# Performance work log

Measured on AMD Instinct MI355X. Metric: run time of the kernel, lower is better.

## Reference

```python
import jax, jax.numpy as jnp
import numpy as np
from jax import lax

B, N, HID = 2, 1024, 2048
H, D, HKV = 32, 64, 8
GROUPS = H // HKV
CHUNK = 64
MAG = 0.5
GATE_NORM = 16.0


def setup_inputs() -> dict:
    key = jax.random.key(0)
    ks = jax.random.split(key, 5)
    hidden_states = jax.random.normal(ks[0], (B, N, HID), jnp.float32)
    Wq = jax.random.normal(ks[1], (HID, H * D), jnp.float32) * 0.02
    Wk = jax.random.normal(ks[2], (HID, HKV * D), jnp.float32) * 0.02
    Wv = jax.random.normal(ks[3], (HID, HKV * D), jnp.float32) * 0.02
    Wo = jax.random.normal(ks[4], (H * D, HID), jnp.float32) * 0.02
    return {"hidden_states": hidden_states, "Wq": Wq, "Wk": Wk, "Wv": Wv, "Wo": Wo}


def _repeat_kv(x, g):
    # [b, hkv, n, d] -> [b, hkv*g, n, d]
    return jnp.repeat(x, g, axis=1)


def _delta_rule_chunked(q, k, v, beta, chunk):
    """Chunked delta-rule linear attention (DeltaNet-style) with elementwise beta gate."""
    b, h, n, d = q.shape
    nc = n // chunk
    qc, kc, vc, bc = (x.reshape(b, h, nc, chunk, d) for x in (q, k, v, beta))
    k_beta = kc * bc
    v_beta = vc * bc
    # T = (I + tril(k_beta k^T, -1))^{-1}, a unit lower-triangular solve per chunk
    strict = jnp.tril(jnp.ones((chunk, chunk), bool), -1)
    L = jnp.einsum('bhnid,bhnjd->bhnij', k_beta, kc) * strict
    M = L + jnp.eye(chunk, dtype=q.dtype)
    eye = jnp.broadcast_to(jnp.eye(chunk, dtype=q.dtype), M.shape)
    T = jax.scipy.linalg.solve_triangular(M, eye, lower=True, unit_diagonal=True)
    u = jnp.einsum('bhnij,bhnjd->bhnid', T, v_beta)   # pseudo-values
    w = jnp.einsum('bhnij,bhnjd->bhnid', T, k_beta)   # pseudo-keys
    causal = jnp.tril(jnp.ones((chunk, chunk), bool))

    def step(S, xs):
        qi, ki, ui, wi = xs  # each [b, h, chunk, d]; S: [b, h, d, d]
        u_p = ui - jnp.einsum('bhcd,bhde->bhce', wi, S)
        attn = jnp.einsum('bhid,bhjd->bhij', qi, ki) * causal
        o = jnp.einsum('bhcd,bhde->bhce', qi, S) + jnp.einsum('bhij,bhjd->bhid', attn, u_p)
        S_new = S + jnp.einsum('bhcd,bhce->bhde', ki, u_p)
        return S_new, o

    xs = tuple(jnp.moveaxis(x, 2, 0) for x in (qc, kc, u, w))  # [nc, b, h, chunk, d]
    S0 = jnp.zeros((b, h, d, d), q.dtype)
    S_final, o = lax.scan(step, S0, xs)
    o = jnp.moveaxis(o, 0, 2).reshape(b, h, n, d)
    return o, S_final


def reference(hidden_states, Wq, Wk, Wv, Wo):
    b, n, _ = hidden_states.shape
    q = hidden_states @ Wq            # [b, n, H*D]
    k = hidden_states @ Wk            # [b, n, HKV*D]
    v = hidden_states @ Wv            # [b, n, HKV*D]
    g = k  # AdaptiveAvgPool1d(512 -> 512) is the identity here

    qh = q.reshape(b, n, H, D).transpose(0, 2, 1, 3)      # [b, H, n, D]
    kh = k.reshape(b, n, HKV, D).transpose(0, 2, 1, 3)    # [b, HKV, n, D]
    vh = v.reshape(b, n, HKV, D).transpose(0, 2, 1, 3)
    gh = g.reshape(b, n, HKV, D).transpose(0, 2, 1, 3)
    k_rep = _repeat_kv(kh, GROUPS)
    v_rep = _repeat_kv(vh, GROUPS)
    g_rep = _repeat_kv(gh, GROUPS)

    # linear-attention branch: softmax feature maps + log-sigmoid gate
    ql = jax.nn.softmax(qh, axis=-1).astype(jnp.float32)
    kl = jax.nn.softmax(k_rep, axis=-1).astype(jnp.float32)
    gl = (jax.nn.log_sigmoid(g_rep) / GATE_NORM).astype(jnp.float32)
    o_lin, _ = _delta_rule_chunked(ql, kl, v_rep.astype(jnp.float32), gl, CHUNK)
    o_lin = o_lin.transpose(0, 2, 1, 3).reshape(b, n, H * D) @ Wo

    # base (vanilla causal) attention branch
    scale = 1.0 / np.sqrt(D).astype(np.float32)
    scores = jnp.einsum('bhid,bhjd->bhij', qh, k_rep) * scale
    causal = jnp.tril(jnp.ones((n, n), bool))
    scores = jnp.where(causal, scores, jnp.finfo(scores.dtype).min)
    attn_weights = jax.nn.softmax(scores, axis=-1)
    o_base = jnp.einsum('bhij,bhjd->bhid', attn_weights, v_rep)
    o_base = o_base.transpose(0, 2, 1, 3).reshape(b, n, H * D) @ Wo

    out = MAG * o_lin + (1.0 - MAG) * o_base
    return out, attn_weights
```

## Files before the change

kernel.cpp:

```cpp
#include <hip/hip_runtime.h>
#include <hip/hip_bf16.h>

constexpr int Bc = 2, Nc = 1024, HIDc = 2048, Hc = 32, Dc = 64, HKVc = 8, NCc = 16;

typedef unsigned short bfu;
typedef __attribute__((ext_vector_type(8))) short frag_ab;
typedef __attribute__((ext_vector_type(4))) float frag_cd;

__device__ __forceinline__ bfu f2bf(float f) {
  unsigned int u = __float_as_uint(f);
  unsigned int r = u + 0x7fffu + ((u >> 16) & 1u);
  return (bfu)(r >> 16);
}
__device__ __forceinline__ ushort4 pack4(float4 v) {
  ushort4 r; r.x = f2bf(v.x); r.y = f2bf(v.y); r.z = f2bf(v.z); r.w = f2bf(v.w);
  return r;
}

__device__ __forceinline__ void gl16(const bfu* g, bfu* l) {
  __builtin_amdgcn_global_load_lds(
      (const __attribute__((address_space(1))) void*)g,
      (__attribute__((address_space(3))) void*)l, 16, 0, 0);
}

__global__ __launch_bounds__(256) void cast_bf16_k(
    const float* __restrict__ in, bfu* __restrict__ out)
{
  const size_t i = ((size_t)blockIdx.x * 256 + threadIdx.x) * 4;
  *(ushort4*)(out + i) = pack4(*(const float4*)(in + i));
}

__global__ __launch_bounds__(256) void transpose_cast_k(
    const float* __restrict__ W, bfu* __restrict__ WT, int K, int N)
{
  __shared__ float t[32][33];
  const int bn = blockIdx.x * 32, bk = blockIdx.y * 32;
  const int x = threadIdx.x & 31, y = threadIdx.x >> 5;
#pragma unroll
  for (int i = 0; i < 32; i += 8)
    t[y + i][x] = W[(size_t)(bk + y + i) * N + bn + x];
  __syncthreads();
#pragma unroll
  for (int i = 0; i < 32; i += 8)
    WT[(size_t)(bn + y + i) * K + bk + x] = f2bf(t[x][y + i]);
}

__global__ __launch_bounds__(256) void transpose_v_k(
    const float* __restrict__ v, bfu* __restrict__ vt)
{
  __shared__ __align__(16) bfu T[64][72];
  const int blk = blockIdx.x;
  const int nt = blk & 15, bh = blk >> 4;
  const int hk = bh & 7, b = bh >> 3;
  const int tid = threadIdx.x;
  const int n = tid >> 2, dv0 = (tid & 3) * 16;
  const float* src = v + ((size_t)(b * Nc + nt * 64 + n) * 8 + hk) * 64 + dv0;
#pragma unroll
  for (int e = 0; e < 16; ++e) T[dv0 + e][n] = f2bf(src[e]);
  __syncthreads();
  const int r = tid >> 3, c = (tid & 7) * 8;
#pragma unroll
  for (int hh = 0; hh < 2; ++hh) {
    const int dv = r + hh * 32;
    *(uint4*)(vt + ((size_t)(bh * 64 + dv)) * 1024 + nt * 64 + c) =
        *(const uint4*)&T[dv][c];
  }
}

__device__ __forceinline__ void gemm128_gl(
    const bfu* __restrict__ A, const bfu* __restrict__ BT,
    float* __restrict__ C, const int Nn, const int m0, const int n0,
    bfu* As, bfu* Bs)
{
  const int tid = threadIdx.x;
  const int wave = tid >> 6, lane = tid & 63;
  const int wm = (wave >> 1) * 64, wn = (wave & 1) * 64;
  const int fm = lane & 15, quad = lane >> 4;
  const int sr = tid >> 2, skc = (tid & 3) * 8;

  frag_cd acc[4][4];
#pragma unroll
  for (int i = 0; i < 4; ++i)
#pragma unroll
    for (int j = 0; j < 4; ++j) acc[i][j] = (frag_cd){0.f, 0.f, 0.f, 0.f};

  const bfu* Ag = A + (size_t)(m0 + sr) * 2048 + skc;
  const bfu* Bg = BT + (size_t)(n0 + sr) * 2048 + skc;
  bfu* Al = As + tid * 8;
  bfu* Bl = Bs + tid * 8;

  for (int k0 = 0; k0 < 2048; k0 += 32) {
    gl16(Ag + k0, Al);
    gl16(Ag + k0 + (size_t)64 * 2048, Al + 64 * 32);
    gl16(Bg + k0, Bl);
    gl16(Bg + k0 + (size_t)64 * 2048, Bl + 64 * 32);
    __syncthreads();
    frag_ab a[4], b[4];
#pragma unroll
    for (int im = 0; im < 4; ++im)
      a[im] = *(const frag_ab*)&As[(size_t)(wm + im * 16 + fm) * 32 + quad * 8];
#pragma unroll
    for (int in = 0; in < 4; ++in)
      b[in] = *(const frag_ab*)&Bs[(size_t)(wn + in * 16 + fm) * 32 + quad * 8];
#pragma unroll
    for (int im = 0; im < 4; ++im)
#pragma unroll
      for (int in = 0; in < 4; ++in)
        acc[im][in] = __builtin_amdgcn_mfma_f32_16x16x32_bf16(
            a[im], b[in], acc[im][in], 0, 0, 0);
    __syncthreads();
  }
#pragma unroll
  for (int im = 0; im < 4; ++im)
#pragma unroll
    for (int in = 0; in < 4; ++in) {
      const int n = n0 + wn + in * 16 + fm;
#pragma unroll
      for (int r = 0; r < 4; ++r) {
        const int m = m0 + wm + im * 16 + quad * 4 + r;
        C[(size_t)m * Nn + n] = acc[im][in][r];
      }
    }
}

__global__ __launch_bounds__(256) void gemm_qkv_k(
    const bfu* __restrict__ A, const bfu* __restrict__ BTq,
    const bfu* __restrict__ BTk, const bfu* __restrict__ BTv,
    float* __restrict__ Cq, float* __restrict__ Ck, float* __restrict__ Cv)
{
  __shared__ __align__(16) bfu As[128 * 32];
  __shared__ __align__(16) bfu Bs[128 * 32];
  int bx = blockIdx.x;
  const bfu* BT; float* C; int Nn;
  if (bx < 16)      { BT = BTq; C = Cq; Nn = 2048; }
  else if (bx < 20) { BT = BTk; C = Ck; Nn = 512; bx -= 16; }
  else              { BT = BTv; C = Cv; Nn = 512; bx -= 20; }
  gemm128_gl(A, BT, C, Nn, blockIdx.y * 128, bx * 128, As, Bs);
}

__global__ __launch_bounds__(256) void gemm_wo_k(
    const bfu* __restrict__ A, const bfu* __restrict__ BT, float* __restrict__ C)
{
  __shared__ __align__(16) bfu As[128 * 32];
  __shared__ __align__(16) bfu Bs[128 * 32];
  gemm128_gl(A, BT, C, 2048, blockIdx.y * 128, blockIdx.x * 128, As, Bs);
}

__global__ __launch_bounds__(256) void gates64_k(
    const float* __restrict__ kin, float* __restrict__ kl, float* __restrict__ gl,
    bfu* __restrict__ k_bf)
{
  const int r = blockIdx.x * 4 + (threadIdx.x >> 6);
  const int lane = threadIdx.x & 63;
  const size_t idx = (size_t)r * 64 + lane;
  const float x = kin[idx];
  k_bf[idx] = f2bf(x);
  float m = x;
#pragma unroll
  for (int o = 32; o > 0; o >>= 1) m = fmaxf(m, __shfl_xor(m, o, 64));
  const float e = __expf(x - m);
  float s = e;
#pragma unroll
  for (int o = 32; o > 0; o >>= 1) s += __shfl_xor(s, o, 64);
  kl[idx] = e / s;
  const float ls = fminf(x, 0.f) - log1pf(__expf(-fabsf(x)));
  gl[idx] = ls * 0.0625f;
}

__global__ __launch_bounds__(256) void chunk_prep_k(
    const float* __restrict__ kl, const float* __restrict__ v,
    const float* __restrict__ gl, float* __restrict__ u_out, float* __restrict__ w_out)
{
  __shared__ __align__(16) float KC[64][68];
  __shared__ float KB[64][65];
  __shared__ float VB[64][65];
  const int blk = blockIdx.x;
  const int c = blk & 15, bh = blk >> 4;
  const int hk = bh & 7, b = bh >> 3;
  const int tid = threadIdx.x;
  for (int x = tid; x < 4096; x += 256) {
    const int i = x >> 6, d = x & 63;
    const size_t src = ((size_t)(b * Nc + c * 64 + i) * 8 + hk) * 64 + d;
    const float kv = kl[src], g = gl[src], vv = v[src];
    KC[d][i] = kv; KB[i][d] = kv * g; VB[i][d] = vv * g;
  }
  __syncthreads();
  const int li = tid >> 2, j0 = (tid & 3) * 16;
  float acc[16];
#pragma unroll
  for (int jj = 0; jj < 16; ++jj) acc[jj] = 0.f;
  for (int d = 0; d < 64; ++d) {
    const float kb = KB[li][d];
    const float4 c0v = *(const float4*)&KC[d][j0];
    const float4 c1v = *(const float4*)&KC[d][j0 + 4];
    const float4 c2v = *(const float4*)&KC[d][j0 + 8];
    const float4 c3v = *(const float4*)&KC[d][j0 + 12];
    acc[0] += kb * c0v.x;  acc[1] += kb * c0v.y;  acc[2] += kb * c0v.z;  acc[3] += kb * c0v.w;
    acc[4] += kb * c1v.x;  acc[5] += kb * c1v.y;  acc[6] += kb * c1v.z;  acc[7] += kb * c1v.w;
    acc[8] += kb * c2v.x;  acc[9] += kb * c2v.y;  acc[10] += kb * c2v.z; acc[11] += kb * c2v.w;
    acc[12] += kb * c3v.x; acc[13] += kb * c3v.y; acc[14] += kb * c3v.z; acc[15] += kb * c3v.w;
  }
  __syncthreads();
#pragma unroll
  for (int jj = 0; jj < 16; ++jj)
    KC[li][j0 + jj] = (j0 + jj < li) ? acc[jj] : 0.f;
  __syncthreads();
  if (tid < 128) {
    const int d = tid & 63;
    float (*X)[65] = (tid < 64) ? VB : KB;
    for (int i = 1; i < 64; ++i) {
      float a2 = X[i][d];
      for (int j = 0; j < i; ++j) a2 -= KC[i][j] * X[j][d];
      X[i][d] = a2;
    }
  }
  __syncthreads();
  for (int x = tid; x < 4096; x += 256) {
    u_out[(size_t)blk * 4096 + x] = VB[x >> 6][x & 63];
    w_out[(size_t)blk * 4096 + x] = KB[x >> 6][x & 63];
  }
}

__global__ __launch_bounds__(512) void scan_k(
    const float* __restrict__ u_ps, const float* __restrict__ w_ps,
    const float* __restrict__ kl, float* __restrict__ u_p, float* __restrict__ S_pre)
{
  __shared__ __align__(16) float S[64][68];
  __shared__ __align__(16) float kw[64][68];
  __shared__ __align__(16) float kt[64][68];
  __shared__ __align__(16) float up[64][68];
  const int blk = blockIdx.x;
  const int hk = blk & 7, b = blk >> 3;
  const int t = threadIdx.x;
  const int row = t >> 3;
  const int c0 = (t & 7) * 8;
  for (int x = t; x < 4096; x += 512) S[x >> 6][x & 63] = 0.f;
  __syncthreads();
  for (int c = 0; c < 16; ++c) {
    const size_t cb = ((size_t)blk * 16 + c) * 4096;
    float upre[8];
    {
      const float* ug = u_ps + cb + row * 64 + c0;
#pragma unroll
      for (int j = 0; j < 8; ++j) upre[j] = ug[j];
    }
    for (int x = t; x < 4096; x += 512) {
      const int i = x >> 6, d = x & 63;
      S_pre[cb + x] = S[i][d];
      kw[i][d] = w_ps[cb + x];
      kt[i][d] = kl[((size_t)(b * Nc + c * 64 + i) * 8 + hk) * 64 + d];
    }
    __syncthreads();
    {
      float acc[8];
#pragma unroll
      for (int j = 0; j < 8; ++j) acc[j] = upre[j];
      for (int e4 = 0; e4 < 64; e4 += 4) {
        const float4 wv4 = *(const float4*)&kw[row][e4];
#pragma unroll
        for (int ee = 0; ee < 4; ++ee) {
          const float wv = ((const float*)&wv4)[ee];
          const float4 s0 = *(const float4*)&S[e4 + ee][c0];
          const float4 s1 = *(const float4*)&S[e4 + ee][c0 + 4];
          acc[0] -= wv * s0.x; acc[1] -= wv * s0.y;
          acc[2] -= wv * s0.z; acc[3] -= wv * s0.w;
          acc[4] -= wv * s1.x; acc[5] -= wv * s1.y;
          acc[6] -= wv * s1.z; acc[7] -= wv * s1.w;
        }
      }
      const float4 o0 = make_float4(acc[0], acc[1], acc[2], acc[3]);
      const float4 o1 = make_float4(acc[4], acc[5], acc[6], acc[7]);
      *(float4*)&up[row][c0] = o0;
      *(float4*)&up[row][c0 + 4] = o1;
      float* upg = u_p + cb + row * 64 + c0;
      *(float4*)upg = o0;
      *(float4*)(upg + 4) = o1;
    }
    __syncthreads();
    {
      float sacc[8];
      {
        const float4 s0 = *(const float4*)&S[row][c0];
        const float4 s1 = *(const float4*)&S[row][c0 + 4];
        sacc[0] = s0.x; sacc[1] = s0.y; sacc[2] = s0.z; sacc[3] = s0.w;
        sacc[4] = s1.x; sacc[5] = s1.y; sacc[6] = s1.z; sacc[7] = s1.w;
      }
      for (int i = 0; i < 64; ++i) {
        const float kv = kt[i][row];
        const float4 u0 = *(const float4*)&up[i][c0];
        const float4 u1 = *(const float4*)&up[i][c0 + 4];
        sacc[0] += kv * u0.x; sacc[1] += kv * u0.y;
        sacc[2] += kv * u0.z; sacc[3] += kv * u0.w;
        sacc[4] += kv * u1.x; sacc[5] += kv * u1.y;
        sacc[6] += kv * u1.z; sacc[7] += kv * u1.w;
      }
      *(float4*)&S[row][c0] = make_float4(sacc[0], sacc[1], sacc[2], sacc[3]);
      *(float4*)&S[row][c0 + 4] = make_float4(sacc[4], sacc[5], sacc[6], sacc[7]);
    }
    __syncthreads();
  }
}

__global__ __launch_bounds__(256) void olin_k(
    const float* __restrict__ qraw, const float* __restrict__ kl,
    const float* __restrict__ upb, const float* __restrict__ S_pre,
    float* __restrict__ o_comb)
{
  __shared__ float Q[64][65];
  __shared__ __align__(16) float Bb[64][68];
  __shared__ float At[64][65];
  const int blk = blockIdx.x;
  const int c = blk & 15, bh = blk >> 4;
  const int h = bh & 31, b = bh >> 5, hk = h >> 2;
  const int tid = threadIdx.x;
  const int i = tid >> 2, d0 = (tid & 3) * 16;
  for (int x = tid; x < 4096; x += 256) {
    const int r = x >> 6, d = x & 63;
    Q[r][d] = qraw[((size_t)(b * Nc + c * 64 + r) * 32 + h) * 64 + d];
    Bb[d][r] = kl[((size_t)(b * Nc + c * 64 + r) * 8 + hk) * 64 + d];
  }
  __syncthreads();
  {
    float mx = -1e30f;
#pragma unroll
    for (int j = 0; j < 16; ++j) mx = fmaxf(mx, Q[i][d0 + j]);
#pragma unroll
    for (int o = 1; o < 4; o <<= 1) mx = fmaxf(mx, __shfl_xor(mx, o, 64));
    float ev[16];
    float sum = 0.f;
#pragma unroll
    for (int j = 0; j < 16; ++j) { ev[j] = __expf(Q[i][d0 + j] - mx); sum += ev[j]; }
#pragma unroll
    for (int o = 1; o < 4; o <<= 1) sum += __shfl_xor(sum, o, 64);
    const float inv = 1.f / sum;
#pragma unroll
    for (int j = 0; j < 16; ++j) Q[i][d0 + j] = ev[j] * inv;
  }
  __syncthreads();
  {
    float a[16];
#pragma unroll
    for (int j = 0; j < 16; ++j) a[j] = 0.f;
    for (int d = 0; d < 64; ++d) {
      const float qv = Q[i][d];
      const float4 b0 = *(const float4*)&Bb[d][d0];
      const float4 b1 = *(const float4*)&Bb[d][d0 + 4];
      const float4 b2 = *(const float4*)&Bb[d][d0 + 8];
      const float4 b3 = *(const float4*)&Bb[d][d0 + 12];
      a[0] += qv * b0.x;  a[1] += qv * b0.y;  a[2] += qv * b0.z;  a[3] += qv * b0.w;
      a[4] += qv * b1.x;  a[5] += qv * b1.y;  a[6] += qv * b1.z;  a[7] += qv * b1.w;
      a[8] += qv * b2.x;  a[9] += qv * b2.y;  a[10] += qv * b2.z; a[11] += qv * b2.w;
      a[12] += qv * b3.x; a[13] += qv * b3.y; a[14] += qv * b3.z; a[15] += qv * b3.w;
    }
#pragma unroll
    for (int j = 0; j < 16; ++j) At[i][d0 + j] = (d0 + j <= i) ? a[j] : 0.f;
  }
  __syncthreads();
  const size_t cb = ((size_t)(b * 8 + hk) * 16 + c) * 4096;
  for (int x = tid; x < 4096; x += 256) Bb[x >> 6][x & 63] = S_pre[cb + x];
  __syncthreads();
  float o[16];
#pragma unroll
  for (int j = 0; j < 16; ++j) o[j] = 0.f;
  for (int e = 0; e < 64; ++e) {
    const float qv = Q[i][e];
#pragma unroll
    for (int j = 0; j < 16; ++j) o[j] += qv * Bb[e][d0 + j];
  }
  __syncthreads();
  for (int x = tid; x < 4096; x += 256) Bb[x >> 6][x & 63] = upb[cb + x];
  __syncthreads();
  for (int j2 = 0; j2 < 64; ++j2) {
    const float av = At[i][j2];
#pragma unroll
    for (int j = 0; j < 16; ++j) o[j] += av * Bb[j2][d0 + j];
  }
  float* oc = o_comb + ((size_t)(b * Nc + c * 64 + i) * 32 + h) * 64 + d0;
#pragma unroll
  for (int j = 0; j < 16; ++j) oc[j] = 0.5f * o[j];
}

template <int LDK>
__device__ __forceinline__ void stage_tile(
    const bfu* __restrict__ g, size_t row_stride, bfu* dst, int tid)
{
  const int xr = tid >> 3;
  const int xc = (tid & 7) * 8;
#pragma unroll
  for (int hh = 0; hh < 2; ++hh) {
    const int row = xr + hh * 32;
    *(uint4*)&dst[(size_t)row * LDK + xc] =
        *(const uint4*)(g + (size_t)row * row_stride + xc);
  }
}

__global__ __launch_bounds__(256) void ml_mfma_k(
    const bfu* __restrict__ qbf, const bfu* __restrict__ kbf,
    float* __restrict__ mbuf, float* __restrict__ lbuf)
{
  constexpr int LDK = 72;
  __shared__ __align__(16) bfu Qt[64 * LDK];
  __shared__ __align__(16) bfu Kt[64 * LDK];
  __shared__ float mred[4][64];
  __shared__ float lred[4][64];
  const int blk = blockIdx.x;
  const int ib = blk & 15, bh = blk >> 4;
  const int h = bh & 31, b = bh >> 5, hk = h >> 2;
  const int tid = threadIdx.x;
  const int wave = tid >> 6, lane = tid & 63;
  const int fm = lane & 15, quad = lane >> 4;
  const int wj = wave * 16;

  stage_tile<LDK>(qbf + ((size_t)(b * Nc + ib * 64) * 32 + h) * 64,
                  (size_t)32 * 64, Qt, tid);
  __syncthreads();
  frag_ab qb[4][2];
#pragma unroll
  for (int in = 0; in < 4; ++in)
#pragma unroll
    for (int kk = 0; kk < 2; ++kk)
      qb[in][kk] = *(const frag_ab*)&Qt[(size_t)(in * 16 + fm) * LDK + kk * 32 + quad * 8];

  float m[4], l[4];
#pragma unroll
  for (int in = 0; in < 4; ++in) { m[in] = -1e30f; l[in] = 0.f; }

  for (int jt = 0; jt <= ib; ++jt) {
    __syncthreads();
    stage_tile<LDK>(kbf + ((size_t)(b * Nc + jt * 64) * 8 + hk) * 64,
                    (size_t)8 * 64, Kt, tid);
    __syncthreads();
    frag_ab ka[2];
    ka[0] = *(const frag_ab*)&Kt[(size_t)(wj + fm) * LDK + quad * 8];
    ka[1] = *(const frag_ab*)&Kt[(size_t)(wj + fm) * LDK + 32 + quad * 8];
    const bool diag = (jt == ib);
#pragma unroll
    for (int in = 0; in < 4; ++in) {
      frag_cd acc = (frag_cd){0.f, 0.f, 0.f, 0.f};
      acc = __builtin_amdgcn_mfma_f32_16x16x32_bf16(ka[0], qb[in][0], acc, 0, 0, 0);
      acc = __builtin_amdgcn_mfma_f32_16x16x32_bf16(ka[1], qb[in][1], acc, 0, 0, 0);
      const int iloc = in * 16 + fm;
      float sv[4];
      bool vd[4];
      float tm = -1e30f;
#pragma unroll
      for (int r = 0; r < 4; ++r) {
        const int jloc = wj + quad * 4 + r;
        vd[r] = !diag || (jloc <= iloc);
        sv[r] = acc[r] * 0.125f;
        if (vd[r]) tm = fmaxf(tm, sv[r]);
      }
      const float mn = fmaxf(m[in], tm);
      float lsum = 0.f;
#pragma unroll
      for (int r = 0; r < 4; ++r)
        if (vd[r]) lsum += __expf(sv[r] - mn);
      l[in] = l[in] * __expf(m[in] - mn) + lsum;
      m[in] = mn;
    }
  }
#pragma unroll
  for (int in = 0; in < 4; ++in) {
    float mm = m[in], ll = l[in];
#pragma unroll
    for (int off = 16; off < 64; off <<= 1) {
      const float mo = __shfl_xor(mm, off, 64);
      const float lo = __shfl_xor(ll, off, 64);
      const float mn = fmaxf(mm, mo);
      ll = ll * __expf(mm - mn) + lo * __expf(mo - mn);
      mm = mn;
    }
    if (quad == 0) { mred[wave][in * 16 + fm] = mm; lred[wave][in * 16 + fm] = ll; }
  }
  __syncthreads();
  if (tid < 64) {
    float M = -1e30f;
#pragma unroll
    for (int w = 0; w < 4; ++w) M = fmaxf(M, mred[w][tid]);
    float L = 0.f;
#pragma unroll
    for (int w = 0; w < 4; ++w) L += lred[w][tid] * __expf(mred[w][tid] - M);
    const size_t rowi = (size_t)(b * 32 + h) * 1024 + ib * 64 + tid;
    mbuf[rowi] = M;
    lbuf[rowi] = L;
  }
}

__global__ __launch_bounds__(256) void pv_mfma_k(
    const bfu* __restrict__ qbf, const bfu* __restrict__ kbf,
    const bfu* __restrict__ vtbf, const float* __restrict__ mbuf,
    const float* __restrict__ lbuf, float* __restrict__ attn,
    const float* __restrict__ o_comb, bfu* __restrict__ oc_bf)
{
  constexpr int LDK = 72;
  __shared__ __align__(16) bfu Qt[64 * LDK];
  __shared__ __align__(16) bfu Kt[64 * LDK];
  __shared__ __align__(16) bfu Vt[64 * LDK];
  __shared__ __align__(16) bfu Pmat[64 * LDK];
  const int blk = blockIdx.x;
  const int ib = blk & 15, bh = blk >> 4;
  const int h = bh & 31, b = bh >> 5, hk = h >> 2;
  const int tid = threadIdx.x;
  const int wave = tid >> 6, lane = tid & 63;
  const int fm = lane & 15, quad = lane >> 4;
  const int wj = wave * 16;
  const int im0 = wave * 16;

  stage_tile<LDK>(qbf + ((size_t)(b * Nc + ib * 64) * 32 + h) * 64,
                  (size_t)32 * 64, Qt, tid);
  __syncthreads();
  frag_ab qb[4][2];
#pragma unroll
  for (int in = 0; in < 4; ++in)
#pragma unroll
    for (int kk = 0; kk < 2; ++kk)
      qb[in][kk] = *(const frag_ab*)&Qt[(size_t)(in * 16 + fm) * LDK + kk * 32 + quad * 8];

  float mi[4], il[4];
#pragma unroll
  for (int in = 0; in < 4; ++in) {
    const size_t rowi = (size_t)(b * 32 + h) * 1024 + ib * 64 + in * 16 + fm;
    mi[in] = mbuf[rowi];
    il[in] = 1.f / lbuf[rowi];
  }

  float* arow0 = attn + ((size_t)(b * 32 + h) * 1024 + ib * 64) * 1024;

  frag_cd o[4];
#pragma unroll
  for (int in = 0; in < 4; ++in) o[in] = (frag_cd){0.f, 0.f, 0.f, 0.f};

  for (int jt = 0; jt <= ib; ++jt) {
    __syncthreads();
    stage_tile<LDK>(kbf + ((size_t)(b * Nc + jt * 64) * 8 + hk) * 64,
                    (size_t)8 * 64, Kt, tid);
    stage_tile<LDK>(vtbf + (size_t)(b * 8 + hk) * 64 * 1024 + jt * 64,
                    (size_t)1024, Vt, tid);
    __syncthreads();
    frag_ab ka[2];
    ka[0] = *(const frag_ab*)&Kt[(size_t)(wj + fm) * LDK + quad * 8];
    ka[1] = *(const frag_ab*)&Kt[(size_t)(wj + fm) * LDK + 32 + quad * 8];
    const bool diag = (jt == ib);
#pragma unroll
    for (int in = 0; in < 4; ++in) {
      frag_cd acc = (frag_cd){0.f, 0.f, 0.f, 0.f};
      acc = __builtin_amdgcn_mfma_f32_16x16x32_bf16(ka[0], qb[in][0], acc, 0, 0, 0);
      acc = __builtin_amdgcn_mfma_f32_16x16x32_bf16(ka[1], qb[in][1], acc, 0, 0, 0);
      const int iloc = in * 16 + fm;
      float p[4];
#pragma unroll
      for (int r = 0; r < 4; ++r) {
        const int jloc = wj + quad * 4 + r;
        const bool vdr = !diag || (jloc <= iloc);
        p[r] = vdr ? __expf(acc[r] * 0.125f - mi[in]) * il[in] : 0.f;
      }
      *(float4*)(arow0 + (size_t)iloc * 1024 + jt * 64 + wj + quad * 4) =
          make_float4(p[0], p[1], p[2], p[3]);
      ushort4 w;
      w.x = f2bf(p[0]); w.y = f2bf(p[1]); w.z = f2bf(p[2]); w.w = f2bf(p[3]);
      *(ushort4*)&Pmat[(size_t)iloc * LDK + wj + quad * 4] = w;
    }
    __syncthreads();
    frag_ab pa[2];
    pa[0] = *(const frag_ab*)&Pmat[(size_t)(im0 + fm) * LDK + quad * 8];
    pa[1] = *(const frag_ab*)&Pmat[(size_t)(im0 + fm) * LDK + 32 + quad * 8];
#pragma unroll
    for (int in = 0; in < 4; ++in) {
      frag_ab vb0 = *(const frag_ab*)&Vt[(size_t)(in * 16 + fm) * LDK + quad * 8];
      frag_ab vb1 = *(const frag_ab*)&Vt[(size_t)(in * 16 + fm) * LDK + 32 + quad * 8];
      o[in] = __builtin_amdgcn_mfma_f32_16x16x32_bf16(pa[0], vb0, o[in], 0, 0, 0);
      o[in] = __builtin_amdgcn_mfma_f32_16x16x32_bf16(pa[1], vb1, o[in], 0, 0, 0);
    }
  }
  for (int jt2 = ib + 1; jt2 < 16; ++jt2) {
    const float4 z = make_float4(0.f, 0.f, 0.f, 0.f);
    for (int x = tid; x < 1024; x += 256) {
      const int row = x >> 4, c4 = (x & 15) * 4;
      *(float4*)(arow0 + (size_t)row * 1024 + jt2 * 64 + c4) = z;
    }
  }
#pragma unroll
  for (int in = 0; in < 4; ++in)
#pragma unroll
    for (int r = 0; r < 4; ++r) {
      const int i = im0 + quad * 4 + r;
      const size_t idx = ((size_t)(b * Nc + ib * 64 + i) * 32 + h) * 64 + in * 16 + fm;
      oc_bf[idx] = f2bf(o_comb[idx] + 0.5f * o[in][r]);
    }
}

extern "C" void kernel_launch(void* const* d_in, const int* in_sizes, int n_in,
                              void* d_out, int out_size, void* d_ws, size_t ws_size,
                              hipStream_t stream) {
  const float* hs = (const float*)d_in[0];
  const float* Wq = (const float*)d_in[1];
  const float* Wk = (const float*)d_in[2];
  const float* Wv = (const float*)d_in[3];
  const float* Wo = (const float*)d_in[4];
  float* out = (float*)d_out;
  float* attn = out + (size_t)Bc * Nc * HIDc;

  float* ws = (float*)d_ws;
  float* q_raw  = ws;
  float* k_raw  = q_raw + 4194304;
  float* v_raw  = k_raw + 1048576;
  float* kl     = v_raw + 1048576;
  float* gl     = kl + 1048576;
  float* u_ps   = gl + 1048576;
  float* w_ps   = u_ps + 2097152;
  float* upb    = w_ps + 2097152;
  float* S_pre  = upb + 2097152;
  float* o_comb = S_pre + 2097152;
  float* mbuf   = o_comb + 4194304;
  float* lbuf   = mbuf + 65536;
  bfu* bstart = (bfu*)(lbuf + 65536);
  bfu* hs_bf  = bstart;
  bfu* WqT    = hs_bf + 4194304;
  bfu* WkT    = WqT + 4194304;
  bfu* WvT    = WkT + 1048576;
  bfu* WoT    = WvT + 1048576;
  bfu* oc_bf  = WoT + 4194304;
  bfu* q_bf   = hs_bf;
  bfu* k_bf   = WqT;
  bfu* vt_bf  = WqT + 1048576;

  cast_bf16_k<<<4096, 256, 0, stream>>>(hs, hs_bf);
  transpose_cast_k<<<dim3(64, 64), 256, 0, stream>>>(Wq, WqT, 2048, 2048);
  transpose_cast_k<<<dim3(16, 64), 256, 0, stream>>>(Wk, WkT, 2048, 512);
  transpose_cast_k<<<dim3(16, 64), 256, 0, stream>>>(Wv, WvT, 2048, 512);
  transpose_cast_k<<<dim3(64, 64), 256, 0, stream>>>(Wo, WoT, 2048, 2048);
  gemm_qkv_k<<<dim3(24, 16), 256, 0, stream>>>(hs_bf, WqT, WkT, WvT,
                                               q_raw, k_raw, v_raw);
  cast_bf16_k<<<4096, 256, 0, stream>>>(q_raw, q_bf);
  gates64_k<<<4096, 256, 0, stream>>>(k_raw, kl, gl, k_bf);
  transpose_v_k<<<256, 256, 0, stream>>>(v_raw, vt_bf);
  chunk_prep_k<<<256, 256, 0, stream>>>(kl, v_raw, gl, u_ps, w_ps);
  scan_k<<<16, 512, 0, stream>>>(u_ps, w_ps, kl, upb, S_pre);
  olin_k<<<1024, 256, 0, stream>>>(q_raw, kl, upb, S_pre, o_comb);
  ml_mfma_k<<<1024, 256, 0, stream>>>(q_bf, k_bf, mbuf, lbuf);
  pv_mfma_k<<<1024, 256, 0, stream>>>(q_bf, k_bf, vt_bf, mbuf, lbuf, attn,
                                      o_comb, oc_bf);
  gemm_wo_k<<<dim3(16, 16), 256, 0, stream>>>(oc_bf, WoT, out);
}
```

Measured before the change: 735.0 us.

## Split scan state by value columns and block the triangular solve

The sequential chunk scan now splits the 64 value columns of the state S into four independent 16-column slices, one per block. This raises the grid from 16 to 64 blocks, each still iterating over the chunks. The chunk_prep forward substitution is reorganised into 16-row blocks, so the off-diagonal updates run across all 256 threads and only the small diagonal blocks stay serial on 128 threads. Each scan block now loads the full w and k tiles redundantly, which adds global traffic.

Result: faster. 676.7 us (-7.9%).

```diff
diff --git a/kernel.cpp b/kernel.cpp
--- a/kernel.cpp
+++ b/kernel.cpp
@@ -205,97 +205,92 @@
   for (int jj = 0; jj < 16; ++jj)
     KC[li][j0 + jj] = (j0 + jj < li) ? acc[jj] : 0.f;
   __syncthreads();
-  if (tid < 128) {
-    const int d = tid & 63;
-    float (*X)[65] = (tid < 64) ? VB : KB;
-    for (int i = 1; i < 64; ++i) {
-      float a2 = X[i][d];
-      for (int j = 0; j < i; ++j) a2 -= KC[i][j] * X[j][d];
-      X[i][d] = a2;
-    }
-  }
-  __syncthreads();
+  for (int r0 = 0; r0 < 64; r0 += 16) {
+    if (r0 > 0) {
+      for (int p = tid; p < 2048; p += 256) {
+        const int ii = p >> 7, dc = p & 127;
+        float (*X)[65] = (dc < 64) ? VB : KB;
+        const int d = dc & 63;
+        float a2 = X[r0 + ii][d];
+        for (int j = 0; j < r0; ++j) a2 -= KC[r0 + ii][j] * X[j][d];
+        X[r0 + ii][d] = a2;
+      }
+      __syncthreads();
+    }
+    if (tid < 128) {
+      const int d = tid & 63;
+      float (*X)[65] = (tid < 64) ? VB : KB;
+      for (int i = r0 + 1; i < r0 + 16; ++i) {
+        float a2 = X[i][d];
+        for (int j = r0; j < i; ++j) a2 -= KC[i][j] * X[j][d];
+        X[i][d] = a2;
+      }
+    }
+    __syncthreads();
+  }
   for (int x = tid; x < 4096; x += 256) {
     u_out[(size_t)blk * 4096 + x] = VB[x >> 6][x & 63];
     w_out[(size_t)blk * 4096 + x] = KB[x >> 6][x & 63];
   }
 }
 
-__global__ __launch_bounds__(512) void scan_k(
+__global__ __launch_bounds__(256) void scan_k(
     const float* __restrict__ u_ps, const float* __restrict__ w_ps,
     const float* __restrict__ kl, float* __restrict__ u_p, float* __restrict__ S_pre)
 {
-  __shared__ __align__(16) float S[64][68];
+  __shared__ __align__(16) float S[64][20];
+  __shared__ __align__(16) float up[64][20];
   __shared__ __align__(16) float kw[64][68];
   __shared__ __align__(16) float kt[64][68];
-  __shared__ __align__(16) float up[64][68];
   const int blk = blockIdx.x;
-  const int hk = blk & 7, b = blk >> 3;
+  const int cg = blk & 3;
+  const int bh = blk >> 2;
+  const int hk = bh & 7, b = bh >> 3;
   const int t = threadIdx.x;
-  const int row = t >> 3;
-  const int c0 = (t & 7) * 8;
-  for (int x = t; x < 4096; x += 512) S[x >> 6][x & 63] = 0.f;
+  const int row = t >> 2;
+  const int c0 = (t & 3) * 4;
+  const int cbase = cg * 16;
+  for (int x = t; x < 1024; x += 256) S[x >> 4][x & 15] = 0.f;
   __syncthreads();
   for (int c = 0; c < 16; ++c) {
-    const size_t cb = ((size_t)blk * 16 + c) * 4096;
-    float upre[8];
+    const size_t cb = ((size_t)bh * 16 + c) * 4096;
+    const float4 upre = *(const float4*)(u_ps + cb + row * 64 + cbase + c0);
+    for (int x = t; x < 1024; x += 256) {
+      const int i = x >> 4, d4 = (x & 15) * 4;
+      *(float4*)&kw[i][d4] = *(const float4*)(w_ps + cb + i * 64 + d4);
+      *(float4*)&kt[i][d4] =
+          *(const float4*)(kl + ((size_t)(b * Nc + c * 64 + i) * 8 + hk) * 64 + d4);
+    }
+    for (int x = t; x < 1024; x += 256) {
+      const int i = x >> 4, cc = x & 15;
+      S_pre[cb + i * 64 + cbase + cc] = S[i][cc];
+    }
+    __syncthreads();
     {
-      const float* ug = u_ps + cb + row * 64 + c0;
-#pragma unroll
-      for (int j = 0; j < 8; ++j) upre[j] = ug[j];
-    }
-    for (int x = t; x < 4096; x += 512) {
-      const int i = x >> 6, d = x & 63;
-      S_pre[cb + x] = S[i][d];
-      kw[i][d] = w_ps[cb + x];
-      kt[i][d] = kl[((size_t)(b * Nc + c * 64 + i) * 8 + hk) * 64 + d];
-    }
-    __syncthreads();
-    {
-      float acc[8];
-#pragma unroll
-      for (int j = 0; j < 8; ++j) acc[j] = upre[j];
+      float a0 = upre.x, a1 = upre.y, a2 = upre.z, a3 = upre.w;
       for (int e4 = 0; e4 < 64; e4 += 4) {
         const float4 wv4 = *(const float4*)&kw[row][e4];
 #pragma unroll
         for (int ee = 0; ee < 4; ++ee) {
           const float wv = ((const float*)&wv4)[ee];
-          const float4 s0 = *(const float4*)&S[e4 + ee][c0];
-          const float4 s1 = *(const float4*)&S[e4 + ee][c0 + 4];
-          acc[0] -= wv * s0.x; acc[1] -= wv * s0.y;
-          acc[2] -= wv * s0.z; acc[3] -= wv * s0.w;
-          acc[4] -= wv * s1.x; acc[5] -= wv * s1.y;
-          acc[6] -= wv * s1.z; acc[7] -= wv * s1.w;
+          const float4 sv = *(const float4*)&S[e4 + ee][c0];
+          a0 -= wv * sv.x; a1 -= wv * sv.y; a2 -= wv * sv.z; a3 -= wv * sv.w;
         }
       }
-      const float4 o0 = make_float4(acc[0], acc[1], acc[2], acc[3]);
-      const float4 o1 = make_float4(acc[4], acc[5], acc[6], acc[7]);
-      *(float4*)&up[row][c0] = o0;
-      *(float4*)&up[row][c0 + 4] = o1;
-      float* upg = u_p + cb + row * 64 + c0;
-      *(float4*)upg = o0;
-      *(float4*)(upg + 4) = o1;
+      const float4 o = make_float4(a0, a1, a2, a3);
+      *(float4*)&up[row][c0] = o;
+      *(float4*)(u_p + cb + row * 64 + cbase + c0) = o;
     }
     __syncthreads();
     {
-      float sacc[8];
-      {
-        const float4 s0 = *(const float4*)&S[row][c0];
-        const float4 s1 = *(const float4*)&S[row][c0 + 4];
-        sacc[0] = s0.x; sacc[1] = s0.y; sacc[2] = s0.z; sacc[3] = s0.w;
-        sacc[4] = s1.x; sacc[5] = s1.y; sacc[6] = s1.z; sacc[7] = s1.w;
-      }
+      const float4 sv = *(const float4*)&S[row][c0];
+      float s0 = sv.x, s1 = sv.y, s2 = sv.z, s3 = sv.w;
       for (int i = 0; i < 64; ++i) {
         const float kv = kt[i][row];
-        const float4 u0 = *(const float4*)&up[i][c0];
-        const float4 u1 = *(const float4*)&up[i][c0 + 4];
-        sacc[0] += kv * u0.x; sacc[1] += kv * u0.y;
-        sacc[2] += kv * u0.z; sacc[3] += kv * u0.w;
-        sacc[4] += kv * u1.x; sacc[5] += kv * u1.y;
-        sacc[6] += kv * u1.z; sacc[7] += kv * u1.w;
+        const float4 uv = *(const float4*)&up[i][c0];
+        s0 += kv * uv.x; s1 += kv * uv.y; s2 += kv * uv.z; s3 += kv * uv.w;
       }
-      *(float4*)&S[row][c0] = make_float4(sacc[0], sacc[1], sacc[2], sacc[3]);
-      *(float4*)&S[row][c0 + 4] = make_float4(sacc[4], sacc[5], sacc[6], sacc[7]);
+      *(float4*)&S[row][c0] = make_float4(s0, s1, s2, s3);
     }
     __syncthreads();
   }
@@ -635,7 +630,7 @@
   gates64_k<<<4096, 256, 0, stream>>>(k_raw, kl, gl, k_bf);
   transpose_v_k<<<256, 256, 0, stream>>>(v_raw, vt_bf);
   chunk_prep_k<<<256, 256, 0, stream>>>(kl, v_raw, gl, u_ps, w_ps);
-  scan_k<<<16, 512, 0, stream>>>(u_ps, w_ps, kl, upb, S_pre);
+  scan_k<<<64, 256, 0, stream>>>(u_ps, w_ps, kl, upb, S_pre);
   olin_k<<<1024, 256, 0, stream>>>(q_raw, kl, upb, S_pre, o_comb);
   ml_mfma_k<<<1024, 256, 0, stream>>>(q_bf, k_bf, mbuf, lbuf);
   pv_mfma_k<<<1024, 256, 0, stream>>>(q_bf, k_bf, vt_bf, mbuf, lbuf, attn,
```
